# Kernel optimization log

Hardware: AMD Instinct MI355X
Metric: run time of the kernel (lower is better)

## Reference

```python
import jax, jax.numpy as jnp
import numpy as np

N = 50000      # num_nodes
SEQ = 52       # seq_len (weeks)
FIN = 16       # in_channels
H = 128        # hidden_dim
E = 800000     # num edges (before self-loops)
NEG_SLOPE = 0.2


def setup_inputs() -> dict:
    key = jax.random.key(0)
    ks = jax.random.split(key, 10)
    return {
        "x_seq": jax.random.normal(ks[0], (SEQ, N, FIN), jnp.float32),
        "edge_index": jax.random.randint(ks[1], (2, E), 0, N),
        "Wg": jax.random.normal(ks[2], (FIN, H), jnp.float32) * 0.1,       # GAT linear (no bias on lin in PyG default path; bias added at end)
        "att_src": jax.random.normal(ks[3], (H,), jnp.float32) * 0.1,
        "att_dst": jax.random.normal(ks[4], (H,), jnp.float32) * 0.1,
        "bias_g": jnp.zeros((H,), jnp.float32),
        "W_ih": jax.random.normal(ks[5], (3 * H, H), jnp.float32) * 0.05,  # GRUCell input weights (r,z,n order)
        "W_hh": jax.random.normal(ks[6], (3 * H, H), jnp.float32) * 0.05,
        "b_ih": jnp.zeros((3 * H,), jnp.float32),
        "b_hh": jnp.zeros((3 * H,), jnp.float32),
        "W_fc": jax.random.normal(ks[7], (1, H), jnp.float32) * 0.1,
        "b_fc": jnp.zeros((1,), jnp.float32),
    }


def _gat(x, src, dst, Wg, att_src, att_dst, bias_g):
    # x: [N, FIN] -> xp: [N, H]
    xp = x @ Wg
    a_s = xp @ att_src  # [N]
    a_d = xp @ att_dst  # [N]
    e = jax.nn.leaky_relu(a_s[src] + a_d[dst], NEG_SLOPE)          # [E+N] edge scores
    m = jax.ops.segment_max(e, dst, num_segments=N)                # softmax over incoming edges per dst
    w = jnp.exp(e - m[dst])
    denom = jax.ops.segment_sum(w, dst, num_segments=N)
    alpha = w / denom[dst]
    out = jax.ops.segment_sum(alpha[:, None] * xp[src], dst, num_segments=N)  # [N, H]
    return out + bias_g


def _gru_cell(x, h, W_ih, W_hh, b_ih, b_hh):
    gi = x @ W_ih.T + b_ih  # [N, 3H]
    gh = h @ W_hh.T + b_hh
    i_r, i_z, i_n = jnp.split(gi, 3, axis=1)
    h_r, h_z, h_n = jnp.split(gh, 3, axis=1)
    r = jax.nn.sigmoid(i_r + h_r)
    z = jax.nn.sigmoid(i_z + h_z)
    n = jnp.tanh(i_n + r * h_n)
    return (1.0 - z) * n + z * h


def reference(x_seq, edge_index, Wg, att_src, att_dst, bias_g, W_ih, W_hh, b_ih, b_hh, W_fc, b_fc):
    # PyG GATConv add_self_loops=True
    loop = jnp.arange(N)
    src = jnp.concatenate([edge_index[0], loop])
    dst = jnp.concatenate([edge_index[1], loop])

    def step(h, xt):
        spatial = jax.nn.relu(_gat(xt, src, dst, Wg, att_src, att_dst, bias_g))
        h_new = _gru_cell(spatial, h, W_ih, W_hh, b_ih, b_hh)
        return h_new, None

    h0 = jnp.zeros((N, H), jnp.float32)
    hT, _ = jax.lax.scan(step, h0, x_seq)
    return hT @ W_fc.T + b_fc  # [N, 1]
```

## Files before the change

### kernel.cpp

```cpp
#include <hip/hip_runtime.h>
#include <math.h>

#define NN 50000
#define SEQ 52
#define FIN 16
#define HD 128
#define NEG_SLOPE 0.2f

typedef short bf16x8 __attribute__((ext_vector_type(8)));
typedef float f32x16 __attribute__((ext_vector_type(16)));

__device__ __forceinline__ short f2bf(float x) {
    unsigned u = __float_as_uint(x);
    u += 0x7fffu + ((u >> 16) & 1u);
    return (short)(u >> 16);
}
__device__ __forceinline__ float b2f(short s) {
    return __uint_as_float(((unsigned)(unsigned short)s) << 16);
}

__global__ void deg_init_kernel(int* deg, int n) {
    int i = blockIdx.x * blockDim.x + threadIdx.x;
    if (i < n) deg[i] = 1;
}

__global__ void deg_count_kernel(const int* __restrict__ dst, int* deg, int e) {
    int i = blockIdx.x * blockDim.x + threadIdx.x;
    if (i < e) atomicAdd(&deg[dst[i]], 1);
}

__global__ __launch_bounds__(1024) void scan_kernel(const int* __restrict__ deg,
                                                    int* row_ptr, int n) {
    __shared__ int buf[1024];
    __shared__ int carry;
    int tid = threadIdx.x;
    if (tid == 0) carry = 0;
    __syncthreads();
    for (int base = 0; base < n; base += 1024) {
        int i = base + tid;
        int v = (i < n) ? deg[i] : 0;
        buf[tid] = v;
        __syncthreads();
        for (int off = 1; off < 1024; off <<= 1) {
            int t = (tid >= off) ? buf[tid - off] : 0;
            __syncthreads();
            buf[tid] += t;
            __syncthreads();
        }
        if (i < n) row_ptr[i] = carry + buf[tid] - v;
        __syncthreads();
        if (tid == 1023) carry += buf[1023];
        __syncthreads();
    }
    if (tid == 0) row_ptr[n] = carry;
}

__global__ void selfloop_kernel(const int* __restrict__ row_ptr, int* cursor,
                                int* col, int n) {
    int i = blockIdx.x * blockDim.x + threadIdx.x;
    if (i < n) {
        int p = row_ptr[i];
        col[p] = i;
        cursor[i] = p + 1;
    }
}

__global__ void scatter_kernel(const int* __restrict__ src, const int* __restrict__ dst,
                               int* cursor, int* col, int e) {
    int i = blockIdx.x * blockDim.x + threadIdx.x;
    if (i < e) {
        int p = atomicAdd(&cursor[dst[i]], 1);
        col[p] = src[i];
    }
}

__global__ void wpack_kernel(const float* __restrict__ Wi, const float* __restrict__ Wh,
                             short* __restrict__ wfrag) {
    int idx = blockIdx.x * blockDim.x + threadIdx.x;
    if (idx >= 3 * 4 * 8 * 4 * 64) return;
    int lane = idx & 63;
    int which = (idx >> 6) & 3;
    int ks = (idx >> 8) & 7;
    int slab = (idx >> 11) & 3;
    int g = idx >> 13;
    int col = slab * 32 + (lane & 31);
    int kcol = ks * 16 + (lane >> 5) * 8;
    const float* Wsrc = (which < 2) ? Wi : Wh;
    const float* row = Wsrc + (size_t)(g * HD + col) * HD + kcol;
    short* dstp = wfrag + (size_t)idx * 8;
    bool lo = (which & 1);
#pragma unroll
    for (int e = 0; e < 8; ++e) {
        float v = row[e];
        short hi = f2bf(v);
        dstp[e] = lo ? f2bf(v - b2f(hi)) : hi;
    }
}


__global__ __launch_bounds__(256) void xp_kernel(
    const float* __restrict__ x, const float* __restrict__ Wg,
    const float* __restrict__ att_src, const float* __restrict__ att_dst,
    unsigned* __restrict__ xpb, float* __restrict__ a_s, float* __restrict__ a_d, int n) {
    int wave = (blockIdx.x * blockDim.x + threadIdx.x) >> 6;
    int lane = threadIdx.x & 63;
    if (wave >= n) return;
    const float* xr = x + (size_t)wave * FIN;
    float xv[FIN];
#pragma unroll
    for (int k = 0; k < FIN; ++k) xv[k] = xr[k];
    int c0 = 2 * lane, c1 = 2 * lane + 1;
    float v0 = 0.f, v1 = 0.f;
#pragma unroll
    for (int k = 0; k < FIN; ++k) {
        v0 += xv[k] * Wg[k * HD + c0];
        v1 += xv[k] * Wg[k * HD + c1];
    }
    unsigned p = (unsigned)(unsigned short)f2bf(v0) |
                 ((unsigned)(unsigned short)f2bf(v1) << 16);
    xpb[(size_t)wave * 64 + lane] = p;
    float s = v0 * att_src[c0] + v1 * att_src[c1];
    float d = v0 * att_dst[c0] + v1 * att_dst[c1];
#pragma unroll
    for (int off = 32; off; off >>= 1) {
        s += __shfl_xor(s, off);
        d += __shfl_xor(d, off);
    }
    if (lane == 0) { a_s[wave] = s; a_d[wave] = d; }
}

__global__ __launch_bounds__(256) void gat_kernel(
    const int* __restrict__ row_ptr, const int* __restrict__ col,
    const float* __restrict__ a_s, const float* __restrict__ a_d,
    const short* __restrict__ xpb, const float* __restrict__ bias_g,
    float* __restrict__ spatial, int n) {
    int wave = (blockIdx.x * blockDim.x + threadIdx.x) >> 6;
    int lane = threadIdx.x & 63;
    if (wave >= n) return;
    int start = row_ptr[wave], end = row_ptr[wave + 1];
    int eg = lane >> 4;
    int fg = lane & 15;
    float ad = a_d[wave];
    float acc[8] = {0.f, 0.f, 0.f, 0.f, 0.f, 0.f, 0.f, 0.f};
    float denom = 0.f;
    for (int i = start + eg; i < end; i += 4) {
        int s = col[i];
        float e = a_s[s] + ad;
        e = (e > 0.f) ? e : NEG_SLOPE * e;
        float wgt = __expf(e);
        denom += wgt;
        bf16x8 row = *(const bf16x8*)(xpb + (size_t)s * HD + fg * 8);
#pragma unroll
        for (int j = 0; j < 8; ++j) acc[j] += wgt * b2f(row[j]);
    }
    denom += __shfl_xor(denom, 16);
    denom += __shfl_xor(denom, 32);
#pragma unroll
    for (int j = 0; j < 8; ++j) {
        acc[j] += __shfl_xor(acc[j], 16);
        acc[j] += __shfl_xor(acc[j], 32);
    }
    float inv = 1.f / denom;
#pragma unroll
    for (int jj = 0; jj < 2; ++jj) {
        int f = fg * 8 + eg * 2 + jj;
        float o = acc[eg * 2 + jj] * inv + bias_g[f];
        spatial[(size_t)wave * HD + f] = fmaxf(o, 0.f);
    }
}

__global__ __launch_bounds__(256, 2) void gru_mfma_kernel(
    const float* __restrict__ spatial, float* __restrict__ h,
    const short* __restrict__ wfrag,
    const float* __restrict__ b_ih, const float* __restrict__ b_hh, int n) {
    __shared__ bf16x8 sSH[512];
    __shared__ bf16x8 sSL[512];
    __shared__ bf16x8 sHH[512];
    __shared__ bf16x8 sHL[512];

    int t = threadIdx.x;
    int lane = t & 63;
    int w = t >> 6;
    int n0 = blockIdx.x * 32;

#pragma unroll
    for (int q = 0; q < 2; ++q) {
        int ks = w * 2 + q;
        int row = n0 + (lane & 31);
        if (row >= n) row = n - 1;
        int kcol = ks * 16 + (lane >> 5) * 8;
        const float* sp = spatial + (size_t)row * HD + kcol;
        const float* hp = h + (size_t)row * HD + kcol;
        float s8[8], h8[8];
        *(float4*)(s8) = *(const float4*)(sp);
        *(float4*)(s8 + 4) = *(const float4*)(sp + 4);
        *(float4*)(h8) = *(const float4*)(hp);
        *(float4*)(h8 + 4) = *(const float4*)(hp + 4);
        bf16x8 sh, sl, hh, hl;
#pragma unroll
        for (int j = 0; j < 8; ++j) {
            short a = f2bf(s8[j]);
            sh[j] = a;
            sl[j] = f2bf(s8[j] - b2f(a));
            short b = f2bf(h8[j]);
            hh[j] = b;
            hl[j] = f2bf(h8[j] - b2f(b));
        }
        int li = ks * 64 + lane;
        sSH[li] = sh; sSL[li] = sl; sHH[li] = hh; sHL[li] = hl;
    }
    __syncthreads();

    int j0 = w * 32;
    int cj = lane & 31;
    int kh = lane >> 5;

    f32x16 arz[2], ain, ahn;
#pragma unroll
    for (int r = 0; r < 16; ++r) {
        arz[0][r] = 0.f; arz[1][r] = 0.f; ain[r] = 0.f; ahn[r] = 0.f;
    }

    const short* wb = wfrag + (size_t)w * 16384 + (size_t)lane * 8;

    bf16x8 wv[3][12];
#pragma unroll
    for (int p = 0; p < 2; ++p) {
#pragma unroll
        for (int g = 0; g < 3; ++g) {
#pragma unroll
            for (int q = 0; q < 4; ++q)
                wv[p][g * 4 + q] = *(const bf16x8*)(wb + g * 65536 + p * 2048 + q * 512);
        }
    }

#pragma unroll
    for (int ks = 0; ks < 8; ++ks) {
        int cur = ks % 3;
        if (ks < 6) {
            int nxt = (ks + 2) % 3;
#pragma unroll
            for (int g = 0; g < 3; ++g) {
#pragma unroll
                for (int q = 0; q < 4; ++q)
                    wv[nxt][g * 4 + q] =
                        *(const bf16x8*)(wb + g * 65536 + (ks + 2) * 2048 + q * 512);
            }
        }
        int li = ks * 64 + lane;
        bf16x8 aSH = sSH[li];
        bf16x8 aSL = sSL[li];
        bf16x8 aHH = sHH[li];
        bf16x8 aHL = sHL[li];
#pragma unroll
        for (int g = 0; g < 2; ++g) {
            bf16x8 wih = wv[cur][g * 4 + 0];
            bf16x8 wil = wv[cur][g * 4 + 1];
            bf16x8 whh = wv[cur][g * 4 + 2];
            bf16x8 whl = wv[cur][g * 4 + 3];
            arz[g] = __builtin_amdgcn_mfma_f32_32x32x16_bf16(aSH, wih, arz[g], 0, 0, 0);
            arz[g] = __builtin_amdgcn_mfma_f32_32x32x16_bf16(aHH, whh, arz[g], 0, 0, 0);
            arz[g] = __builtin_amdgcn_mfma_f32_32x32x16_bf16(aSL, wih, arz[g], 0, 0, 0);
            arz[g] = __builtin_amdgcn_mfma_f32_32x32x16_bf16(aHL, whh, arz[g], 0, 0, 0);
            arz[g] = __builtin_amdgcn_mfma_f32_32x32x16_bf16(aSH, wil, arz[g], 0, 0, 0);
            arz[g] = __builtin_amdgcn_mfma_f32_32x32x16_bf16(aHH, whl, arz[g], 0, 0, 0);
        }
        {
            bf16x8 wih = wv[cur][8];
            bf16x8 wil = wv[cur][9];
            bf16x8 whh = wv[cur][10];
            bf16x8 whl = wv[cur][11];
            ain = __builtin_amdgcn_mfma_f32_32x32x16_bf16(aSH, wih, ain, 0, 0, 0);
            ahn = __builtin_amdgcn_mfma_f32_32x32x16_bf16(aHH, whh, ahn, 0, 0, 0);
            ain = __builtin_amdgcn_mfma_f32_32x32x16_bf16(aSL, wih, ain, 0, 0, 0);
            ahn = __builtin_amdgcn_mfma_f32_32x32x16_bf16(aHL, whh, ahn, 0, 0, 0);
            ain = __builtin_amdgcn_mfma_f32_32x32x16_bf16(aSH, wil, ain, 0, 0, 0);
            ahn = __builtin_amdgcn_mfma_f32_32x32x16_bf16(aHH, whl, ahn, 0, 0, 0);
        }
    }

    int j = j0 + cj;
    float brz0 = b_ih[j] + b_hh[j];
    float brz1 = b_ih[HD + j] + b_hh[HD + j];
    float bin_ = b_ih[2 * HD + j];
    float bhn = b_hh[2 * HD + j];
    const short* hhs = (const short*)sHH;
    const short* hls = (const short*)sHL;
    int ksj = j >> 4, halfj = (j >> 3) & 1, ej = j & 7;

#pragma unroll
    for (int r = 0; r < 16; ++r) {
        int nl = (r & 3) + 8 * (r >> 2) + 4 * kh;
        int node = n0 + nl;
        if (node < n) {
            float rr = 1.f / (1.f + __expf(-(arz[0][r] + brz0)));
            float zz = 1.f / (1.f + __expf(-(arz[1][r] + brz1)));
            float nn2 = tanhf(ain[r] + bin_ + rr * (ahn[r] + bhn));
            int li = (ksj * 64 + nl + 32 * halfj) * 8 + ej;
            float hold = b2f(hhs[li]) + b2f(hls[li]);
            h[(size_t)node * HD + j] = (1.f - zz) * nn2 + zz * hold;
        }
    }
}

__global__ __launch_bounds__(256) void fc_kernel(
    const float* __restrict__ h, const float* __restrict__ W_fc,
    const float* __restrict__ b_fc, float* __restrict__ out, int n) {
    int wave = (blockIdx.x * blockDim.x + threadIdx.x) >> 6;
    int lane = threadIdx.x & 63;
    if (wave >= n) return;
    float v = h[(size_t)wave * HD + lane] * W_fc[lane] +
              h[(size_t)wave * HD + lane + 64] * W_fc[lane + 64];
#pragma unroll
    for (int off = 32; off; off >>= 1) v += __shfl_xor(v, off);
    if (lane == 0) out[wave] = v + b_fc[0];
}

extern "C" void kernel_launch(void* const* d_in, const int* in_sizes, int n_in,
                              void* d_out, int out_size, void* d_ws, size_t ws_size,
                              hipStream_t stream) {
    const float* x_seq   = (const float*)d_in[0];
    const int*   ei      = (const int*)d_in[1];
    const float* Wg      = (const float*)d_in[2];
    const float* att_src = (const float*)d_in[3];
    const float* att_dst = (const float*)d_in[4];
    const float* bias_g  = (const float*)d_in[5];
    const float* W_ih    = (const float*)d_in[6];
    const float* W_hh    = (const float*)d_in[7];
    const float* b_ih    = (const float*)d_in[8];
    const float* b_hh    = (const float*)d_in[9];
    const float* W_fc    = (const float*)d_in[10];
    const float* b_fc    = (const float*)d_in[11];
    float* out = (float*)d_out;

    const int N = NN;
    const int E = in_sizes[1] / 2;
    const int* src = ei;
    const int* dst = ei + E;

    char* w = (char*)d_ws;
    size_t off = 0;
    auto alloc = [&](size_t bytes) {
        char* p = w + off;
        off = (off + bytes + 255) & ~(size_t)255;
        return p;
    };
    int*   deg     = (int*)alloc((size_t)N * 4);
    int*   row_ptr = (int*)alloc((size_t)(N + 1) * 4);
    int*   cursor  = (int*)alloc((size_t)N * 4);
    int*   col     = (int*)alloc((size_t)(E + N) * 4);
    float* a_s     = (float*)alloc((size_t)N * 4);
    float* a_d     = (float*)alloc((size_t)N * 4);
    unsigned* xpb  = (unsigned*)alloc((size_t)N * 64 * 4);
    float* spatial = (float*)alloc((size_t)N * HD * 4);
    float* hbuf    = (float*)alloc((size_t)N * HD * 4);
    short* wfrag   = (short*)alloc((size_t)3 * 4 * 8 * 4 * 64 * 8 * 2);

    hipMemsetAsync(hbuf, 0, (size_t)N * HD * 4, stream);

    deg_init_kernel<<<(N + 255) / 256, 256, 0, stream>>>(deg, N);
    deg_count_kernel<<<(E + 255) / 256, 256, 0, stream>>>(dst, deg, E);
    scan_kernel<<<1, 1024, 0, stream>>>(deg, row_ptr, N);
    selfloop_kernel<<<(N + 255) / 256, 256, 0, stream>>>(row_ptr, cursor, col, N);
    scatter_kernel<<<(E + 255) / 256, 256, 0, stream>>>(src, dst, cursor, col, E);
    wpack_kernel<<<(24576 + 255) / 256, 256, 0, stream>>>(W_ih, W_hh, wfrag);

    int node_wave_blocks = (N * 64 + 255) / 256;
    int gru_blocks = (N + 31) / 32;

    for (int t = 0; t < SEQ; ++t) {
        const float* xt = x_seq + (size_t)t * N * FIN;
        xp_kernel<<<node_wave_blocks, 256, 0, stream>>>(xt, Wg, att_src, att_dst,
                                                        xpb, a_s, a_d, N);
        gat_kernel<<<node_wave_blocks, 256, 0, stream>>>(row_ptr, col, a_s, a_d,
                                                         (const short*)xpb, bias_g,
                                                         spatial, N);
        gru_mfma_kernel<<<gru_blocks, 256, 0, stream>>>(spatial, hbuf, wfrag,
                                                        b_ih, b_hh, N);
    }
    fc_kernel<<<node_wave_blocks, 256, 0, stream>>>(hbuf, W_fc, b_fc, out, N);
}
```

Before: 6.833 ms.

## Fuse GAT aggregation into GRU kernel, writing spatial features directly to LDS

Merges the GAT neighbor-aggregation kernel into the GRU MFMA kernel. Each block now aggregates its 32 nodes with 16-thread groups per node, loading edge indices cooperatively and broadcasting them via shuffles, then writes the bf16 hi/lo split straight into shared memory. This removes the fp32 spatial buffer's global write and read and one launch per timestep. It also swaps in fast-math sigmoid and tanh using __expf and __fdividef, which costs some precision, and the fused kernel may have lower occupancy because of the extra register pressure.

```diff
diff --git a/kernel.cpp b/kernel.cpp
--- a/kernel.cpp
+++ b/kernel.cpp
@@ -129,49 +129,11 @@
     if (lane == 0) { a_s[wave] = s; a_d[wave] = d; }
 }
 
-__global__ __launch_bounds__(256) void gat_kernel(
+__global__ __launch_bounds__(256, 2) void gatgru_kernel(
     const int* __restrict__ row_ptr, const int* __restrict__ col,
     const float* __restrict__ a_s, const float* __restrict__ a_d,
     const short* __restrict__ xpb, const float* __restrict__ bias_g,
-    float* __restrict__ spatial, int n) {
-    int wave = (blockIdx.x * blockDim.x + threadIdx.x) >> 6;
-    int lane = threadIdx.x & 63;
-    if (wave >= n) return;
-    int start = row_ptr[wave], end = row_ptr[wave + 1];
-    int eg = lane >> 4;
-    int fg = lane & 15;
-    float ad = a_d[wave];
-    float acc[8] = {0.f, 0.f, 0.f, 0.f, 0.f, 0.f, 0.f, 0.f};
-    float denom = 0.f;
-    for (int i = start + eg; i < end; i += 4) {
-        int s = col[i];
-        float e = a_s[s] + ad;
-        e = (e > 0.f) ? e : NEG_SLOPE * e;
-        float wgt = __expf(e);
-        denom += wgt;
-        bf16x8 row = *(const bf16x8*)(xpb + (size_t)s * HD + fg * 8);
-#pragma unroll
-        for (int j = 0; j < 8; ++j) acc[j] += wgt * b2f(row[j]);
-    }
-    denom += __shfl_xor(denom, 16);
-    denom += __shfl_xor(denom, 32);
-#pragma unroll
-    for (int j = 0; j < 8; ++j) {
-        acc[j] += __shfl_xor(acc[j], 16);
-        acc[j] += __shfl_xor(acc[j], 32);
-    }
-    float inv = 1.f / denom;
-#pragma unroll
-    for (int jj = 0; jj < 2; ++jj) {
-        int f = fg * 8 + eg * 2 + jj;
-        float o = acc[eg * 2 + jj] * inv + bias_g[f];
-        spatial[(size_t)wave * HD + f] = fmaxf(o, 0.f);
-    }
-}
-
-__global__ __launch_bounds__(256, 2) void gru_mfma_kernel(
-    const float* __restrict__ spatial, float* __restrict__ h,
-    const short* __restrict__ wfrag,
+    float* __restrict__ h, const short* __restrict__ wfrag,
     const float* __restrict__ b_ih, const float* __restrict__ b_hh, int n) {
     __shared__ bf16x8 sSH[512];
     __shared__ bf16x8 sSL[512];
@@ -183,31 +145,103 @@
     int w = t >> 6;
     int n0 = blockIdx.x * 32;
 
+    float h8[2][8];
 #pragma unroll
     for (int q = 0; q < 2; ++q) {
         int ks = w * 2 + q;
         int row = n0 + (lane & 31);
         if (row >= n) row = n - 1;
         int kcol = ks * 16 + (lane >> 5) * 8;
-        const float* sp = spatial + (size_t)row * HD + kcol;
         const float* hp = h + (size_t)row * HD + kcol;
-        float s8[8], h8[8];
-        *(float4*)(s8) = *(const float4*)(sp);
-        *(float4*)(s8 + 4) = *(const float4*)(sp + 4);
-        *(float4*)(h8) = *(const float4*)(hp);
-        *(float4*)(h8 + 4) = *(const float4*)(hp + 4);
-        bf16x8 sh, sl, hh, hl;
+        *(float4*)(h8[q]) = *(const float4*)(hp);
+        *(float4*)(h8[q] + 4) = *(const float4*)(hp + 4);
+    }
+
+    int g = t >> 4;
+    int fg = t & 15;
+    int glane = lane & 0x30;
+
+#pragma unroll
+    for (int nn = 0; nn < 2; ++nn) {
+        int nl = g + nn * 16;
+        int nd = n0 + nl;
+        int sidx = (fg >> 1) * 64 + (fg & 1) * 32 + nl;
+        if (nd < n) {
+            int start = row_ptr[nd], end = row_ptr[nd + 1];
+            float ad = a_d[nd];
+            float acc[8] = {0.f, 0.f, 0.f, 0.f, 0.f, 0.f, 0.f, 0.f};
+            float dpart = 0.f;
+            for (int base = start; base < end; base += 16) {
+                int cnt = end - base;
+                if (cnt > 16) cnt = 16;
+                int s = 0;
+                float wgt = 0.f;
+                if (fg < cnt) {
+                    s = col[base + fg];
+                    float e = a_s[s] + ad;
+                    e = (e > 0.f) ? e : NEG_SLOPE * e;
+                    wgt = __expf(e);
+                }
+                dpart += wgt;
+                for (int k = 0; k < cnt; k += 4) {
+                    int si[4];
+                    float wt[4];
+#pragma unroll
+                    for (int u = 0; u < 4; ++u) {
+                        int c = k + u;
+                        int cc = (c < cnt) ? c : 0;
+                        si[u] = __shfl(s, glane | cc);
+                        wt[u] = __shfl(wgt, glane | cc);
+                        if (c >= cnt) wt[u] = 0.f;
+                    }
+                    bf16x8 r[4];
+#pragma unroll
+                    for (int u = 0; u < 4; ++u)
+                        r[u] = *(const bf16x8*)(xpb + (size_t)si[u] * HD + fg * 8);
+#pragma unroll
+                    for (int u = 0; u < 4; ++u)
+#pragma unroll
+                        for (int j = 0; j < 8; ++j) acc[j] += wt[u] * b2f(r[u][j]);
+                }
+            }
+            dpart += __shfl_xor(dpart, 8);
+            dpart += __shfl_xor(dpart, 4);
+            dpart += __shfl_xor(dpart, 2);
+            dpart += __shfl_xor(dpart, 1);
+            float inv = __fdividef(1.f, dpart);
+            bf16x8 sh, sl;
+#pragma unroll
+            for (int j = 0; j < 8; ++j) {
+                float o = acc[j] * inv + bias_g[fg * 8 + j];
+                o = fmaxf(o, 0.f);
+                short hi = f2bf(o);
+                sh[j] = hi;
+                sl[j] = f2bf(o - b2f(hi));
+            }
+            sSH[sidx] = sh;
+            sSL[sidx] = sl;
+        } else {
+            bf16x8 z;
+#pragma unroll
+            for (int j = 0; j < 8; ++j) z[j] = 0;
+            sSH[sidx] = z;
+            sSL[sidx] = z;
+        }
+    }
+
+#pragma unroll
+    for (int q = 0; q < 2; ++q) {
+        int ks = w * 2 + q;
+        bf16x8 hh, hl;
 #pragma unroll
         for (int j = 0; j < 8; ++j) {
-            short a = f2bf(s8[j]);
-            sh[j] = a;
-            sl[j] = f2bf(s8[j] - b2f(a));
-            short b = f2bf(h8[j]);
+            short b = f2bf(h8[q][j]);
             hh[j] = b;
-            hl[j] = f2bf(h8[j] - b2f(b));
+            hl[j] = f2bf(h8[q][j] - b2f(b));
         }
         int li = ks * 64 + lane;
-        sSH[li] = sh; sSL[li] = sl; sHH[li] = hh; sHL[li] = hl;
+        sHH[li] = hh;
+        sHL[li] = hl;
     }
     __syncthreads();
 
@@ -227,10 +261,10 @@
 #pragma unroll
     for (int p = 0; p < 2; ++p) {
 #pragma unroll
-        for (int g = 0; g < 3; ++g) {
+        for (int gg = 0; gg < 3; ++gg) {
 #pragma unroll
             for (int q = 0; q < 4; ++q)
-                wv[p][g * 4 + q] = *(const bf16x8*)(wb + g * 65536 + p * 2048 + q * 512);
+                wv[p][gg * 4 + q] = *(const bf16x8*)(wb + gg * 65536 + p * 2048 + q * 512);
         }
     }
 
@@ -240,11 +274,11 @@
         if (ks < 6) {
             int nxt = (ks + 2) % 3;
 #pragma unroll
-            for (int g = 0; g < 3; ++g) {
+            for (int gg = 0; gg < 3; ++gg) {
 #pragma unroll
                 for (int q = 0; q < 4; ++q)
-                    wv[nxt][g * 4 + q] =
-                        *(const bf16x8*)(wb + g * 65536 + (ks + 2) * 2048 + q * 512);
+                    wv[nxt][gg * 4 + q] =
+                        *(const bf16x8*)(wb + gg * 65536 + (ks + 2) * 2048 + q * 512);
             }
         }
         int li = ks * 64 + lane;
@@ -253,17 +287,17 @@
         bf16x8 aHH = sHH[li];
         bf16x8 aHL = sHL[li];
 #pragma unroll
-        for (int g = 0; g < 2; ++g) {
-            bf16x8 wih = wv[cur][g * 4 + 0];
-            bf16x8 wil = wv[cur][g * 4 + 1];
-            bf16x8 whh = wv[cur][g * 4 + 2];
-            bf16x8 whl = wv[cur][g * 4 + 3];
-            arz[g] = __builtin_amdgcn_mfma_f32_32x32x16_bf16(aSH, wih, arz[g], 0, 0, 0);
-            arz[g] = __builtin_amdgcn_mfma_f32_32x32x16_bf16(aHH, whh, arz[g], 0, 0, 0);
-            arz[g] = __builtin_amdgcn_mfma_f32_32x32x16_bf16(aSL, wih, arz[g], 0, 0, 0);
-            arz[g] = __builtin_amdgcn_mfma_f32_32x32x16_bf16(aHL, whh, arz[g], 0, 0, 0);
-            arz[g] = __builtin_amdgcn_mfma_f32_32x32x16_bf16(aSH, wil, arz[g], 0, 0, 0);
-            arz[g] = __builtin_amdgcn_mfma_f32_32x32x16_bf16(aHH, whl, arz[g], 0, 0, 0);
+        for (int gg = 0; gg < 2; ++gg) {
+            bf16x8 wih = wv[cur][gg * 4 + 0];
+            bf16x8 wil = wv[cur][gg * 4 + 1];
+            bf16x8 whh = wv[cur][gg * 4 + 2];
+            bf16x8 whl = wv[cur][gg * 4 + 3];
+            arz[gg] = __builtin_amdgcn_mfma_f32_32x32x16_bf16(aSH, wih, arz[gg], 0, 0, 0);
+            arz[gg] = __builtin_amdgcn_mfma_f32_32x32x16_bf16(aHH, whh, arz[gg], 0, 0, 0);
+            arz[gg] = __builtin_amdgcn_mfma_f32_32x32x16_bf16(aSL, wih, arz[gg], 0, 0, 0);
+            arz[gg] = __builtin_amdgcn_mfma_f32_32x32x16_bf16(aHL, whh, arz[gg], 0, 0, 0);
+            arz[gg] = __builtin_amdgcn_mfma_f32_32x32x16_bf16(aSH, wil, arz[gg], 0, 0, 0);
+            arz[gg] = __builtin_amdgcn_mfma_f32_32x32x16_bf16(aHH, whl, arz[gg], 0, 0, 0);
         }
         {
             bf16x8 wih = wv[cur][8];
@@ -293,9 +327,11 @@
         int nl = (r & 3) + 8 * (r >> 2) + 4 * kh;
         int node = n0 + nl;
         if (node < n) {
-            float rr = 1.f / (1.f + __expf(-(arz[0][r] + brz0)));
-            float zz = 1.f / (1.f + __expf(-(arz[1][r] + brz1)));
-            float nn2 = tanhf(ain[r] + bin_ + rr * (ahn[r] + bhn));
+            float rr = __fdividef(1.f, 1.f + __expf(-(arz[0][r] + brz0)));
+            float zz = __fdividef(1.f, 1.f + __expf(-(arz[1][r] + brz1)));
+            float u = ain[r] + bin_ + rr * (ahn[r] + bhn);
+            float ex = __expf(2.f * u);
+            float nn2 = 1.f - __fdividef(2.f, ex + 1.f);
             int li = (ksj * 64 + nl + 32 * halfj) * 8 + ej;
             float hold = b2f(hhs[li]) + b2f(hls[li]);
             h[(size_t)node * HD + j] = (1.f - zz) * nn2 + zz * hold;
@@ -352,7 +388,6 @@
     float* a_s     = (float*)alloc((size_t)N * 4);
     float* a_d     = (float*)alloc((size_t)N * 4);
     unsigned* xpb  = (unsigned*)alloc((size_t)N * 64 * 4);
-    float* spatial = (float*)alloc((size_t)N * HD * 4);
     float* hbuf    = (float*)alloc((size_t)N * HD * 4);
     short* wfrag   = (short*)alloc((size_t)3 * 4 * 8 * 4 * 64 * 8 * 2);
 
@@ -366,17 +401,15 @@
     wpack_kernel<<<(24576 + 255) / 256, 256, 0, stream>>>(W_ih, W_hh, wfrag);
 
     int node_wave_blocks = (N * 64 + 255) / 256;
-    int gru_blocks = (N + 31) / 32;
+    int fused_blocks = (N + 31) / 32;
 
     for (int t = 0; t < SEQ; ++t) {
         const float* xt = x_seq + (size_t)t * N * FIN;
         xp_kernel<<<node_wave_blocks, 256, 0, stream>>>(xt, Wg, att_src, att_dst,
                                                         xpb, a_s, a_d, N);
-        gat_kernel<<<node_wave_blocks, 256, 0, stream>>>(row_ptr, col, a_s, a_d,
-                                                         (const short*)xpb, bias_g,
-                                                         spatial, N);
-        gru_mfma_kernel<<<gru_blocks, 256, 0, stream>>>(spatial, hbuf, wfrag,
-                                                        b_ih, b_hh, N);
+        gatgru_kernel<<<fused_blocks, 256, 0, stream>>>(row_ptr, col, a_s, a_d,
+                                                        (const short*)xpb, bias_g,
+                                                        hbuf, wfrag, b_ih, b_hh, N);
     }
     fc_kernel<<<node_wave_blocks, 256, 0, stream>>>(hbuf, W_fc, b_fc, out, N);
 }
```

New measurement: 6.299 ms. -7.8%, faster.
